# Performance work log

Hardware: AMD Instinct MI355X
Metric: run time of the kernel (lower is better)

Reference implementation:

```python
import jax, jax.numpy as jnp
import numpy as np

N = 100000
E = 3200000
IN_C, HID_C, OUT_C = 128, 16, 1


def setup_inputs() -> dict:
    key = jax.random.key(0)
    k1, k2, k3, k4, k5, k6 = jax.random.split(key, 6)
    x = jax.random.normal(k1, (N, IN_C), dtype=jnp.float32)
    edge_index = jax.random.randint(k2, (2, E), 0, N, dtype=jnp.int64)
    # Glorot-style init like PyG GCNConv
    W1 = jax.random.normal(k3, (IN_C, HID_C), dtype=jnp.float32) / np.sqrt(IN_C)
    b1 = jnp.zeros((HID_C,), dtype=jnp.float32)
    W2 = jax.random.normal(k4, (HID_C, OUT_C), dtype=jnp.float32) / np.sqrt(HID_C)
    b2 = jnp.zeros((OUT_C,), dtype=jnp.float32)
    return {"x": x, "edge_index": edge_index, "W1": W1, "b1": b1, "W2": W2, "b2": b2}


def _gcn_conv(x, W, b, src, dst, norm):
    # Linear transform first (PyG default flow: transform then aggregate)
    h = x @ W                                  # [N, C_out]
    msg = h[src] * norm[:, None]               # gather + edge-wise scale, [E+N, C_out]
    out = jax.ops.segment_sum(msg, dst, num_segments=N)  # scatter-add, [N, C_out]
    return out + b


def reference(x, edge_index, W1, b1, W2, b2):
    # GCNConv: add self-loops, symmetric normalization D^-1/2 A D^-1/2
    loop = jnp.arange(N, dtype=edge_index.dtype)
    src = jnp.concatenate([edge_index[0], loop])   # [E+N]
    dst = jnp.concatenate([edge_index[1], loop])   # [E+N]
    deg = jax.ops.segment_sum(jnp.ones_like(dst, dtype=x.dtype), dst, num_segments=N)
    dinv = jnp.where(deg > 0, jax.lax.rsqrt(deg), 0.0)
    norm = dinv[src] * dinv[dst]                   # [E+N]

    h = _gcn_conv(x, W1, b1, src, dst, norm)
    h = jax.nn.relu(h)
    # dropout is identity in eval mode (training=False)
    h = _gcn_conv(h, W2, b2, src, dst, norm)
    return jax.nn.sigmoid(h).squeeze()             # [N]
```

## Files before the change

### kernel.cpp

```cpp
#include <hip/hip_runtime.h>
#include <hip/hip_bf16.h>
#include <math.h>

typedef unsigned int u32;

constexpr int N_NODES = 100000;
constexpr int N_EDGES = 3200000;
constexpr int IN_C    = 128;
constexpr int HID_C   = 16;

constexpr int BKT_SHIFT = 11;
constexpr int BKT_NODES = 1 << BKT_SHIFT;
constexpr int NB  = (N_NODES + BKT_NODES - 1) / BKT_NODES;
constexpr int CAP = 67000;
constexpr int EPB = N_EDGES / 256;
constexpr int MAXE = (EPB + 1023) / 1024;
constexpr int K_SEG = 8;
constexpr int QW = 4;

__global__ void k_zero(u32* __restrict__ cursor) {
    int i = threadIdx.x;
    if (i < NB) cursor[i] = 0u;
}

__global__ __launch_bounds__(1024) void k_bucket(const int* __restrict__ src,
                                                 const int* __restrict__ dst,
                                                 u32* __restrict__ cursor,
                                                 u32* __restrict__ barr) {
    __shared__ u32 cnt4[QW][NB];
    __shared__ u32 lpre4[QW][NB];
    __shared__ u32 cur4[QW][NB];
    __shared__ u32 gbase[NB];
    __shared__ u32 bstart[NB + 1];
    __shared__ u32 ents[EPB];
    const int e0 = blockIdx.x * EPB;
    const int q = threadIdx.x >> 8;
    u32 myD[MAXE], myS[MAXE];
#pragma unroll
    for (int i = 0; i < MAXE; ++i) {
        int r = threadIdx.x + i * 1024;
        if (r < EPB) { myD[i] = (u32)dst[e0 + r]; myS[i] = (u32)src[e0 + r]; }
        else myD[i] = 0xFFFFFFFFu;
    }
    for (int i = threadIdx.x; i < QW * NB; i += 1024) ((u32*)cnt4)[i] = 0u;
    __syncthreads();
#pragma unroll
    for (int i = 0; i < MAXE; ++i)
        if (myD[i] != 0xFFFFFFFFu) atomicAdd(&cnt4[q][myD[i] >> BKT_SHIFT], 1u);
    __syncthreads();
    if (threadIdx.x == 0) {
        u32 t = 0;
        for (int b = 0; b < NB; ++b) {
            bstart[b] = t;
            for (int qq = 0; qq < QW; ++qq) { lpre4[qq][b] = t; t += cnt4[qq][b]; }
        }
        bstart[NB] = t;
    }
    __syncthreads();
    if (threadIdx.x < NB)
        gbase[threadIdx.x] = atomicAdd(&cursor[threadIdx.x],
                                       bstart[threadIdx.x + 1] - bstart[threadIdx.x]);
    for (int i = threadIdx.x; i < QW * NB; i += 1024) ((u32*)cur4)[i] = ((u32*)lpre4)[i];
    __syncthreads();
#pragma unroll
    for (int i = 0; i < MAXE; ++i) {
        if (myD[i] == 0xFFFFFFFFu) continue;
        u32 b = myD[i] >> BKT_SHIFT;
        u32 pos = atomicAdd(&cur4[q][b], 1u);
        ents[pos] = ((myD[i] & (BKT_NODES - 1)) << 17) | myS[i];
    }
    __syncthreads();
    for (int i = threadIdx.x; i < EPB; i += 1024) {
        int lo = 0, hi = NB - 1;
        while (lo < hi) { int mid = (lo + hi + 1) >> 1; if (bstart[mid] <= (u32)i) lo = mid; else hi = mid - 1; }
        u32 off = gbase[lo] + ((u32)i - bstart[lo]);
        if (off < (u32)CAP) barr[(size_t)lo * CAP + off] = ents[i];
    }
}

__global__ __launch_bounds__(1024) void k_hist(const u32* __restrict__ barr,
                                               const u32* __restrict__ cursor,
                                               u32* __restrict__ seghist) {
    __shared__ u32 h[BKT_NODES];
    const int b = blockIdx.x / K_SEG, s = blockIdx.x % K_SEG;
    const u32 sz = min(cursor[b], (u32)CAP);
    for (int i = threadIdx.x; i < BKT_NODES; i += blockDim.x) h[i] = 0u;
    __syncthreads();
    const u32 e0 = sz * (u32)s / K_SEG, e1 = sz * (u32)(s + 1) / K_SEG;
    const u32* p = barr + (size_t)b * CAP;
    for (u32 e = e0 + threadIdx.x; e < e1; e += blockDim.x)
        atomicAdd(&h[p[e] >> 17], 1u);
    __syncthreads();
    u32* o = seghist + (size_t)(b * K_SEG + s) * BKT_NODES;
    for (int i = threadIdx.x; i < BKT_NODES; i += blockDim.x) o[i] = h[i];
}

__global__ __launch_bounds__(1024) void k_scan(u32* __restrict__ seghist,
                                               const u32* __restrict__ cursor,
                                               int* __restrict__ rowptr,
                                               float* __restrict__ dinv) {
    __shared__ u32 sa[BKT_NODES], sb[BKT_NODES];
    __shared__ u32 s_bb;
    const int b = blockIdx.x;
    const int nbase = b << BKT_SHIFT;
    if (threadIdx.x == 0) {
        u32 t = 0;
        for (int q = 0; q < b; ++q) t += min(cursor[q], (u32)CAP);
        s_bb = t;
        if (b == NB - 1) rowptr[N_NODES] = (int)(t + min(cursor[b], (u32)CAP));
    }
    for (int n = threadIdx.x; n < BKT_NODES; n += blockDim.x) {
        u32 t = 0;
#pragma unroll
        for (int s = 0; s < K_SEG; ++s) {
            size_t idx = (size_t)(b * K_SEG + s) * BKT_NODES + n;
            u32 v = seghist[idx];
            seghist[idx] = t;
            t += v;
        }
        sa[n] = t;
        if (nbase + n < N_NODES) dinv[nbase + n] = rsqrtf(1.0f + (float)t);
    }
    __syncthreads();
    u32 *pa = sa, *pb = sb;
    for (int off = 1; off < BKT_NODES; off <<= 1) {
        for (int n = threadIdx.x; n < BKT_NODES; n += blockDim.x)
            pb[n] = pa[n] + (n >= off ? pa[n - off] : 0u);
        __syncthreads();
        u32* t = pa; pa = pb; pb = t;
    }
    const u32 bb = s_bb;
    for (int n = threadIdx.x; n < BKT_NODES; n += blockDim.x) {
        u32 excl = bb + (n ? pa[n - 1] : 0u);
        if (nbase + n < N_NODES) rowptr[nbase + n] = (int)excl;
#pragma unroll
        for (int s = 0; s < K_SEG; ++s)
            seghist[(size_t)(b * K_SEG + s) * BKT_NODES + n] += excl;
    }
}

__global__ __launch_bounds__(1024) void k_scatter(const u32* __restrict__ barr,
                                                  const u32* __restrict__ cursor,
                                                  const u32* __restrict__ seghist,
                                                  int* __restrict__ adj) {
    __shared__ u32 cur[BKT_NODES];
    const int b = blockIdx.x / K_SEG, s = blockIdx.x % K_SEG;
    const u32 sz = min(cursor[b], (u32)CAP);
    const u32* sbase = seghist + (size_t)(b * K_SEG + s) * BKT_NODES;
    for (int i = threadIdx.x; i < BKT_NODES; i += blockDim.x) cur[i] = sbase[i];
    __syncthreads();
    const u32 e0 = sz * (u32)s / K_SEG, e1 = sz * (u32)(s + 1) / K_SEG;
    const u32* p = barr + (size_t)b * CAP;
    for (u32 e = e0 + threadIdx.x; e < e1; e += blockDim.x) {
        u32 ent = p[e];
        u32 pos = atomicAdd(&cur[ent >> 17], 1u);
        adj[pos] = (int)(ent & 0x1FFFFu);
    }
}

constexpr int NPB = 16;
constexpr int XPAD = 132;
__global__ __launch_bounds__(256) void k_gemm1(const float* __restrict__ x,
                                               const float* __restrict__ W1,
                                               const float* __restrict__ dinv,
                                               __hip_bfloat16* __restrict__ g1b) {
    __shared__ float sx[NPB * XPAD];
    __shared__ float swT[HID_C * XPAD];
    const int nbase = blockIdx.x * NPB;
    {
        const float4* xs = (const float4*)(x + (size_t)nbase * IN_C);
#pragma unroll
        for (int k = 0; k < 2; ++k) {
            int idx = threadIdx.x + k * 256;
            int row = idx >> 5, col4 = idx & 31;
            float4 v = xs[idx];
            ((float4*)(sx + row * XPAD))[col4] = v;
        }
    }
    for (int t = threadIdx.x; t < IN_C * HID_C; t += 256) {
        int j = t >> 4, c = t & 15;
        swT[c * XPAD + j] = W1[t];
    }
    __syncthreads();

    const int n = threadIdx.x >> 4;
    const int c = threadIdx.x & 15;
    const float4* row = (const float4*)(sx + n * XPAD);
    const float4* wc  = (const float4*)(swT + c * XPAD);
    float acc = 0.f;
#pragma unroll
    for (int j = 0; j < IN_C / 4; ++j) {
        float4 v = row[j];
        float4 w = wc[j];
        acc = fmaf(v.x, w.x, acc);
        acc = fmaf(v.y, w.y, acc);
        acc = fmaf(v.z, w.z, acc);
        acc = fmaf(v.w, w.w, acc);
    }
    const int node = nbase + n;
    g1b[node * HID_C + c] = __float2bfloat16(acc * dinv[node]);
}

__global__ void k_agg1(const int* __restrict__ rowptr, const int* __restrict__ adj,
                       const uint2* __restrict__ g1p,
                       const float* __restrict__ dinv, const float* __restrict__ b1,
                       const float* __restrict__ W2, float* __restrict__ g2) {
    int t = blockIdx.x * blockDim.x + threadIdx.x;
    int g = t >> 2, l = t & 3;
    if (g >= N_NODES) return;
    int base = rowptr[g], end = rowptr[g + 1];
    uint2 sv = g1p[g * 4 + l];
    float a0 = __uint_as_float(sv.x << 16);
    float a1 = __uint_as_float(sv.x & 0xFFFF0000u);
    float a2 = __uint_as_float(sv.y << 16);
    float a3 = __uint_as_float(sv.y & 0xFFFF0000u);
    int k = base;
    for (; k + 4 <= end; k += 4) {
        int s0 = adj[k], s1 = adj[k + 1], s2 = adj[k + 2], s3 = adj[k + 3];
        uint2 v0 = g1p[s0 * 4 + l], v1 = g1p[s1 * 4 + l];
        uint2 v2 = g1p[s2 * 4 + l], v3 = g1p[s3 * 4 + l];
        a0 += __uint_as_float(v0.x << 16);
        a1 += __uint_as_float(v0.x & 0xFFFF0000u);
        a2 += __uint_as_float(v0.y << 16);
        a3 += __uint_as_float(v0.y & 0xFFFF0000u);
        a0 += __uint_as_float(v1.x << 16);
        a1 += __uint_as_float(v1.x & 0xFFFF0000u);
        a2 += __uint_as_float(v1.y << 16);
        a3 += __uint_as_float(v1.y & 0xFFFF0000u);
        a0 += __uint_as_float(v2.x << 16);
        a1 += __uint_as_float(v2.x & 0xFFFF0000u);
        a2 += __uint_as_float(v2.y << 16);
        a3 += __uint_as_float(v2.y & 0xFFFF0000u);
        a0 += __uint_as_float(v3.x << 16);
        a1 += __uint_as_float(v3.x & 0xFFFF0000u);
        a2 += __uint_as_float(v3.y << 16);
        a3 += __uint_as_float(v3.y & 0xFFFF0000u);
    }
    for (; k < end; ++k) {
        uint2 v = g1p[adj[k] * 4 + l];
        a0 += __uint_as_float(v.x << 16);
        a1 += __uint_as_float(v.x & 0xFFFF0000u);
        a2 += __uint_as_float(v.y << 16);
        a3 += __uint_as_float(v.y & 0xFFFF0000u);
    }
    float di = dinv[g];
    float2 ba = ((const float2*)b1)[2 * l], bb = ((const float2*)b1)[2 * l + 1];
    float2 wa = ((const float2*)W2)[2 * l], wb = ((const float2*)W2)[2 * l + 1];
    float h0 = fmaxf(fmaf(a0, di, ba.x), 0.f);
    float h1 = fmaxf(fmaf(a1, di, ba.y), 0.f);
    float h2 = fmaxf(fmaf(a2, di, bb.x), 0.f);
    float h3 = fmaxf(fmaf(a3, di, bb.y), 0.f);
    float part = h0 * wa.x + h1 * wa.y + h2 * wb.x + h3 * wb.y;
    part += __shfl_xor(part, 1);
    part += __shfl_xor(part, 2);
    if (l == 0) g2[g] = part * di;
}

__global__ void k_agg2(const int* __restrict__ rowptr, const int* __restrict__ adj,
                       const float* __restrict__ g2, const float* __restrict__ dinv,
                       const float* __restrict__ b2, float* __restrict__ out) {
    int t = blockIdx.x * blockDim.x + threadIdx.x;
    int g = t >> 2, l = t & 3;
    if (g >= N_NODES) return;
    int base = rowptr[g], end = rowptr[g + 1];
    float acc = (l == 0) ? g2[g] : 0.f;
    for (int k = base + l; k < end; k += 4) acc += g2[adj[k]];
    acc += __shfl_xor(acc, 1);
    acc += __shfl_xor(acc, 2);
    if (l == 0) {
        float v = fmaf(acc, dinv[g], b2[0]);
        out[g] = 1.0f / (1.0f + __expf(-v));
    }
}

extern "C" void kernel_launch(void* const* d_in, const int* in_sizes, int n_in,
                              void* d_out, int out_size, void* d_ws, size_t ws_size,
                              hipStream_t stream) {
    const float* x    = (const float*)d_in[0];
    const int*   edge = (const int*)d_in[1];
    const float* W1   = (const float*)d_in[2];
    const float* b1   = (const float*)d_in[3];
    const float* W2   = (const float*)d_in[4];
    const float* b2   = (const float*)d_in[5];
    float*       out  = (float*)d_out;

    const int* src = edge;
    const int* dst = edge + N_EDGES;

    char* w = (char*)d_ws;
    auto alloc = [&](size_t bytes) { char* r = w; w += (bytes + 255) & ~(size_t)255; return r; };
    u32*   barr       = (u32*)  alloc((size_t)NB * CAP * 4);
    u32*   seghist    = (u32*)  alloc((size_t)NB * K_SEG * BKT_NODES * 4);
    u32*   cursor     = (u32*)  alloc(NB * 4);
    int*   rowptr     = (int*)  alloc((size_t)(N_NODES + 1) * 4);
    float* dinv       = (float*)alloc((size_t)N_NODES * 4);
    int*   adj        = (int*)  alloc((size_t)N_EDGES * 4);
    float*          g2  = (float*)barr;
    __hip_bfloat16* g1b = (__hip_bfloat16*)seghist;
    const uint2*    g1p = (const uint2*)seghist;

    const int gGemm = N_NODES / NPB;
    const int gAgg1 = (N_NODES * 4 + 255) / 256;
    const int gAgg2 = (N_NODES * 4 + 255) / 256;

    hipLaunchKernelGGL(k_zero,    dim3(1),          dim3(64),   0, stream, cursor);
    hipLaunchKernelGGL(k_bucket,  dim3(256),        dim3(1024), 0, stream, src, dst, cursor, barr);
    hipLaunchKernelGGL(k_hist,    dim3(NB * K_SEG), dim3(1024), 0, stream, barr, cursor, seghist);
    hipLaunchKernelGGL(k_scan,    dim3(NB),         dim3(1024), 0, stream, seghist, cursor, rowptr, dinv);
    hipLaunchKernelGGL(k_scatter, dim3(NB * K_SEG), dim3(1024), 0, stream, barr, cursor, seghist, adj);
    hipLaunchKernelGGL(k_gemm1,   dim3(gGemm),      dim3(256),  0, stream, x, W1, dinv, g1b);
    hipLaunchKernelGGL(k_agg1,    dim3(gAgg1),      dim3(256),  0, stream, rowptr, adj, g1p, dinv, b1, W2, g2);
    hipLaunchKernelGGL(k_agg2,    dim3(gAgg2),      dim3(256),  0, stream, rowptr, adj, g2, dinv, b2, out);
}
```

Before: 228.9 us.

## Rework bucket flush, wave-shuffle scan, wider agg1 gathers, more hist segments

New measurement: 232.9 us. No clear change (+1.7%).

```diff
diff --git a/kernel.cpp b/kernel.cpp
--- a/kernel.cpp
+++ b/kernel.cpp
@@ -15,7 +15,7 @@
 constexpr int CAP = 67000;
 constexpr int EPB = N_EDGES / 256;
 constexpr int MAXE = (EPB + 1023) / 1024;
-constexpr int K_SEG = 8;
+constexpr int K_SEG = 16;
 constexpr int QW = 4;
 
 __global__ void k_zero(u32* __restrict__ cursor) {
@@ -70,11 +70,13 @@
         ents[pos] = ((myD[i] & (BKT_NODES - 1)) << 17) | myS[i];
     }
     __syncthreads();
-    for (int i = threadIdx.x; i < EPB; i += 1024) {
-        int lo = 0, hi = NB - 1;
-        while (lo < hi) { int mid = (lo + hi + 1) >> 1; if (bstart[mid] <= (u32)i) lo = mid; else hi = mid - 1; }
-        u32 off = gbase[lo] + ((u32)i - bstart[lo]);
-        if (off < (u32)CAP) barr[(size_t)lo * CAP + off] = ents[i];
+    const int wv = threadIdx.x >> 6, ln = threadIdx.x & 63;
+    for (int b = wv; b < NB; b += 16) {
+        u32 s0 = bstart[b], s1 = bstart[b + 1], gb = gbase[b];
+        for (u32 i = s0 + ln; i < s1; i += 64) {
+            u32 off = gb + (i - s0);
+            if (off < (u32)CAP) barr[(size_t)b * CAP + off] = ents[i];
+        }
     }
 }
 
@@ -99,7 +101,8 @@
                                                const u32* __restrict__ cursor,
                                                int* __restrict__ rowptr,
                                                float* __restrict__ dinv) {
-    __shared__ u32 sa[BKT_NODES], sb[BKT_NODES];
+    __shared__ u32 sa[BKT_NODES];
+    __shared__ u32 wsum[16];
     __shared__ u32 s_bb;
     const int b = blockIdx.x;
     const int nbase = b << BKT_SHIFT;
@@ -109,7 +112,7 @@
         s_bb = t;
         if (b == NB - 1) rowptr[N_NODES] = (int)(t + min(cursor[b], (u32)CAP));
     }
-    for (int n = threadIdx.x; n < BKT_NODES; n += blockDim.x) {
+    for (int n = threadIdx.x; n < BKT_NODES; n += 1024) {
         u32 t = 0;
 #pragma unroll
         for (int s = 0; s < K_SEG; ++s) {
@@ -122,16 +125,35 @@
         if (nbase + n < N_NODES) dinv[nbase + n] = rsqrtf(1.0f + (float)t);
     }
     __syncthreads();
-    u32 *pa = sa, *pb = sb;
-    for (int off = 1; off < BKT_NODES; off <<= 1) {
-        for (int n = threadIdx.x; n < BKT_NODES; n += blockDim.x)
-            pb[n] = pa[n] + (n >= off ? pa[n - off] : 0u);
-        __syncthreads();
-        u32* t = pa; pa = pb; pb = t;
-    }
+    const int lane = threadIdx.x & 63, wv = threadIdx.x >> 6;
+    u32 v0 = sa[2 * threadIdx.x], v1 = sa[2 * threadIdx.x + 1];
+    u32 p = v0 + v1;
+    u32 ip = p;
+#pragma unroll
+    for (int off = 1; off < 64; off <<= 1) {
+        u32 nv = __shfl_up(ip, off);
+        if (lane >= off) ip += nv;
+    }
+    if (lane == 63) wsum[wv] = ip;
+    __syncthreads();
+    if (threadIdx.x < 16) {
+        u32 wx = wsum[threadIdx.x];
+#pragma unroll
+        for (int off = 1; off < 16; off <<= 1) {
+            u32 nv = __shfl_up(wx, off);
+            if ((int)threadIdx.x >= off) wx += nv;
+        }
+        wsum[threadIdx.x] = wx;
+    }
+    __syncthreads();
+    u32 wbase = wv ? wsum[wv - 1] : 0u;
+    u32 epair = wbase + ip - p;
+    sa[2 * threadIdx.x]     = epair + v0;
+    sa[2 * threadIdx.x + 1] = epair + p;
+    __syncthreads();
     const u32 bb = s_bb;
-    for (int n = threadIdx.x; n < BKT_NODES; n += blockDim.x) {
-        u32 excl = bb + (n ? pa[n - 1] : 0u);
+    for (int n = threadIdx.x; n < BKT_NODES; n += 1024) {
+        u32 excl = bb + (n ? sa[n - 1] : 0u);
         if (nbase + n < N_NODES) rowptr[nbase + n] = (int)excl;
 #pragma unroll
         for (int s = 0; s < K_SEG; ++s)
@@ -202,57 +224,88 @@
 }
 
 __global__ void k_agg1(const int* __restrict__ rowptr, const int* __restrict__ adj,
-                       const uint2* __restrict__ g1p,
+                       const uint4* __restrict__ g1q,
                        const float* __restrict__ dinv, const float* __restrict__ b1,
                        const float* __restrict__ W2, float* __restrict__ g2) {
     int t = blockIdx.x * blockDim.x + threadIdx.x;
-    int g = t >> 2, l = t & 3;
+    int g = t >> 1, l = t & 1;
     if (g >= N_NODES) return;
     int base = rowptr[g], end = rowptr[g + 1];
-    uint2 sv = g1p[g * 4 + l];
-    float a0 = __uint_as_float(sv.x << 16);
-    float a1 = __uint_as_float(sv.x & 0xFFFF0000u);
-    float a2 = __uint_as_float(sv.y << 16);
-    float a3 = __uint_as_float(sv.y & 0xFFFF0000u);
+    float a0, a1, a2, a3, a4, a5, a6, a7;
+    {
+        uint4 sv = g1q[g * 2 + l];
+        a0 = __uint_as_float(sv.x << 16);
+        a1 = __uint_as_float(sv.x & 0xFFFF0000u);
+        a2 = __uint_as_float(sv.y << 16);
+        a3 = __uint_as_float(sv.y & 0xFFFF0000u);
+        a4 = __uint_as_float(sv.z << 16);
+        a5 = __uint_as_float(sv.z & 0xFFFF0000u);
+        a6 = __uint_as_float(sv.w << 16);
+        a7 = __uint_as_float(sv.w & 0xFFFF0000u);
+    }
     int k = base;
     for (; k + 4 <= end; k += 4) {
         int s0 = adj[k], s1 = adj[k + 1], s2 = adj[k + 2], s3 = adj[k + 3];
-        uint2 v0 = g1p[s0 * 4 + l], v1 = g1p[s1 * 4 + l];
-        uint2 v2 = g1p[s2 * 4 + l], v3 = g1p[s3 * 4 + l];
+        uint4 v0 = g1q[s0 * 2 + l], v1 = g1q[s1 * 2 + l];
+        uint4 v2 = g1q[s2 * 2 + l], v3 = g1q[s3 * 2 + l];
         a0 += __uint_as_float(v0.x << 16);
         a1 += __uint_as_float(v0.x & 0xFFFF0000u);
         a2 += __uint_as_float(v0.y << 16);
         a3 += __uint_as_float(v0.y & 0xFFFF0000u);
+        a4 += __uint_as_float(v0.z << 16);
+        a5 += __uint_as_float(v0.z & 0xFFFF0000u);
+        a6 += __uint_as_float(v0.w << 16);
+        a7 += __uint_as_float(v0.w & 0xFFFF0000u);
         a0 += __uint_as_float(v1.x << 16);
         a1 += __uint_as_float(v1.x & 0xFFFF0000u);
         a2 += __uint_as_float(v1.y << 16);
         a3 += __uint_as_float(v1.y & 0xFFFF0000u);
+        a4 += __uint_as_float(v1.z << 16);
+        a5 += __uint_as_float(v1.z & 0xFFFF0000u);
+        a6 += __uint_as_float(v1.w << 16);
+        a7 += __uint_as_float(v1.w & 0xFFFF0000u);
         a0 += __uint_as_float(v2.x << 16);
         a1 += __uint_as_float(v2.x & 0xFFFF0000u);
         a2 += __uint_as_float(v2.y << 16);
         a3 += __uint_as_float(v2.y & 0xFFFF0000u);
+        a4 += __uint_as_float(v2.z << 16);
+        a5 += __uint_as_float(v2.z & 0xFFFF0000u);
+        a6 += __uint_as_float(v2.w << 16);
+        a7 += __uint_as_float(v2.w & 0xFFFF0000u);
         a0 += __uint_as_float(v3.x << 16);
         a1 += __uint_as_float(v3.x & 0xFFFF0000u);
         a2 += __uint_as_float(v3.y << 16);
         a3 += __uint_as_float(v3.y & 0xFFFF0000u);
+        a4 += __uint_as_float(v3.z << 16);
+        a5 += __uint_as_float(v3.z & 0xFFFF0000u);
+        a6 += __uint_as_float(v3.w << 16);
+        a7 += __uint_as_float(v3.w & 0xFFFF0000u);
     }
     for (; k < end; ++k) {
-        uint2 v = g1p[adj[k] * 4 + l];
+        uint4 v = g1q[adj[k] * 2 + l];
         a0 += __uint_as_float(v.x << 16);
         a1 += __uint_as_float(v.x & 0xFFFF0000u);
         a2 += __uint_as_float(v.y << 16);
         a3 += __uint_as_float(v.y & 0xFFFF0000u);
+        a4 += __uint_as_float(v.z << 16);
+        a5 += __uint_as_float(v.z & 0xFFFF0000u);
+        a6 += __uint_as_float(v.w << 16);
+        a7 += __uint_as_float(v.w & 0xFFFF0000u);
     }
     float di = dinv[g];
-    float2 ba = ((const float2*)b1)[2 * l], bb = ((const float2*)b1)[2 * l + 1];
-    float2 wa = ((const float2*)W2)[2 * l], wb = ((const float2*)W2)[2 * l + 1];
-    float h0 = fmaxf(fmaf(a0, di, ba.x), 0.f);
-    float h1 = fmaxf(fmaf(a1, di, ba.y), 0.f);
-    float h2 = fmaxf(fmaf(a2, di, bb.x), 0.f);
-    float h3 = fmaxf(fmaf(a3, di, bb.y), 0.f);
-    float part = h0 * wa.x + h1 * wa.y + h2 * wb.x + h3 * wb.y;
+    float4 bA = ((const float4*)b1)[2 * l], bB = ((const float4*)b1)[2 * l + 1];
+    float4 wA = ((const float4*)W2)[2 * l], wB = ((const float4*)W2)[2 * l + 1];
+    float h0 = fmaxf(fmaf(a0, di, bA.x), 0.f);
+    float h1 = fmaxf(fmaf(a1, di, bA.y), 0.f);
+    float h2 = fmaxf(fmaf(a2, di, bA.z), 0.f);
+    float h3 = fmaxf(fmaf(a3, di, bA.w), 0.f);
+    float h4 = fmaxf(fmaf(a4, di, bB.x), 0.f);
+    float h5 = fmaxf(fmaf(a5, di, bB.y), 0.f);
+    float h6 = fmaxf(fmaf(a6, di, bB.z), 0.f);
+    float h7 = fmaxf(fmaf(a7, di, bB.w), 0.f);
+    float part = h0 * wA.x + h1 * wA.y + h2 * wA.z + h3 * wA.w
+               + h4 * wB.x + h5 * wB.y + h6 * wB.z + h7 * wB.w;
     part += __shfl_xor(part, 1);
-    part += __shfl_xor(part, 2);
     if (l == 0) g2[g] = part * di;
 }
 
@@ -278,8 +331,8 @@
                               hipStream_t stream) {
     const float* x    = (const float*)d_in[0];
     const int*   edge = (const int*)d_in[1];
+    const float* b1   = (const float*)d_in[3];
     const float* W1   = (const float*)d_in[2];
-    const float* b1   = (const float*)d_in[3];
     const float* W2   = (const float*)d_in[4];
     const float* b2   = (const float*)d_in[5];
     float*       out  = (float*)d_out;
@@ -297,10 +350,10 @@
     int*   adj        = (int*)  alloc((size_t)N_EDGES * 4);
     float*          g2  = (float*)barr;
     __hip_bfloat16* g1b = (__hip_bfloat16*)seghist;
-    const uint2*    g1p = (const uint2*)seghist;
+    const uint4*    g1q = (const uint4*)seghist;
 
     const int gGemm = N_NODES / NPB;
-    const int gAgg1 = (N_NODES * 4 + 255) / 256;
+    const int gAgg1 = (N_NODES * 2 + 255) / 256;
     const int gAgg2 = (N_NODES * 4 + 255) / 256;
 
     hipLaunchKernelGGL(k_zero,    dim3(1),          dim3(64),   0, stream, cursor);
@@ -309,6 +362,6 @@
     hipLaunchKernelGGL(k_scan,    dim3(NB),         dim3(1024), 0, stream, seghist, cursor, rowptr, dinv);
     hipLaunchKernelGGL(k_scatter, dim3(NB * K_SEG), dim3(1024), 0, stream, barr, cursor, seghist, adj);
     hipLaunchKernelGGL(k_gemm1,   dim3(gGemm),      dim3(256),  0, stream, x, W1, dinv, g1b);
-    hipLaunchKernelGGL(k_agg1,    dim3(gAgg1),      dim3(256),  0, stream, rowptr, adj, g1p, dinv, b1, W2, g2);
+    hipLaunchKernelGGL(k_agg1,    dim3(gAgg1),      dim3(256),  0, stream, rowptr, adj, g1q, dinv, b1, W2, g2);
     hipLaunchKernelGGL(k_agg2,    dim3(gAgg2),      dim3(256),  0, stream, rowptr, adj, g2, dinv, b2, out);
 }
```
